# Kernel optimization log

Hardware: AMD Instinct MI355X
Metric: run time of the kernel (lower is better)

## Reference

```python
import jax, jax.numpy as jnp
import numpy as np

N, E, G = 10000, 40000, 128          # nodes, edges, graphs
NF, EF, H, NH, GD, L = 92, 50, 64, 10, 108, 5  # feat dims, hidden, heads, global dim, layers
EPS = 1e-5

def _lrelu(v):
    return jax.nn.leaky_relu(v, 0.2)

def setup_inputs() -> dict:
    key = jax.random.key(0)
    ks = jax.random.split(key, 24)
    def rn(k, shp, s=0.05):
        return jax.random.normal(k, shp, jnp.float32) * s
    return {
        "x": jax.random.normal(ks[0], (N, NF), jnp.float32),
        "edge_index": jax.random.randint(ks[1], (2, E), 0, N, dtype=jnp.int32),
        "edge_attr": jax.random.normal(ks[2], (E, EF), jnp.float32),
        "batch_idx": jnp.sort(jax.random.randint(ks[3], (N,), 0, G, dtype=jnp.int32)),
        "global_features": jax.random.normal(ks[4], (G, GD), jnp.float32),
        "node_W": rn(ks[5], (NF, H)), "node_b": jnp.zeros((H,), jnp.float32),
        "edge_W": rn(ks[6], (EF, H)), "edge_b": jnp.zeros((H,), jnp.float32),
        "conv_W": rn(ks[7], (L, 2 * H, NH * H)),
        "conv_att": rn(ks[8], (L, NH, 2 * H)),
        "conv_b": jnp.zeros((L, H), jnp.float32),
        "conv_gamma": jnp.ones((L, NH), jnp.float32),
        "conv_beta": jnp.zeros((L, NH), jnp.float32),
        "ga_W1": rn(ks[9], (H + GD, H)), "ga_b1": jnp.zeros((H,), jnp.float32),
        "ga_W2": rn(ks[10], (H, 1)), "ga_b2": jnp.zeros((1,), jnp.float32),
        "out_W1": rn(ks[11], (H, H)), "out_b1": jnp.zeros((H,), jnp.float32),
        "out_W2": rn(ks[12], (H, 1)), "out_b2": jnp.zeros((1,), jnp.float32),
    }

def reference(x, edge_index, edge_attr, batch_idx, global_features,
              node_W, node_b, edge_W, edge_b,
              conv_W, conv_att, conv_b, conv_gamma, conv_beta,
              ga_W1, ga_b1, ga_W2, ga_b2, out_W1, out_b1, out_W2, out_b2):
    row, col = edge_index[0], edge_index[1]
    # embeddings
    h = _lrelu(x @ node_W + node_b)            # [N, H]
    ea = _lrelu(edge_attr @ edge_W + edge_b)   # [E, H]
    initial = h
    inv_std = 1.0 / jnp.sqrt(1.0 + EPS)        # DiffGroupNorm eval: running mean=0, var=1
    for i in range(L):
        xi = jnp.concatenate([h[row], ea], axis=-1)               # [E, 2H]
        xj = jnp.concatenate([h[col], ea], axis=-1)
        hi = _lrelu(xi @ conv_W[i]).reshape(E, NH, H)             # [E, NH, H]
        hj = _lrelu(xj @ conv_W[i]).reshape(E, NH, H)
        alpha = jnp.sum(jnp.concatenate([hi, hj], -1) * conv_att[i][None], -1)  # [E, NH]
        alpha = _lrelu(alpha)
        alpha = alpha * inv_std * conv_gamma[i] + conv_beta[i]
        alpha = jax.nn.softmax(alpha, axis=1)                     # softmax over heads
        msg = (hj * alpha[..., None]).reshape(E, NH * H)
        agg = jax.ops.segment_sum(msg, row, num_segments=N).reshape(N, NH, H)
        h_new = agg.mean(axis=1) + conv_b[i]
        h = h + h_new if i > 0 else h_new
    h = h + initial
    # global attention: softmax over nodes within each graph
    g = global_features[batch_idx]                                 # [N, GD]
    s = _lrelu(jnp.concatenate([h, g], -1) @ ga_W1 + ga_b1)
    score = (s @ ga_W2 + ga_b2)[:, 0]                              # [N]
    smax = jax.ops.segment_max(score, batch_idx, num_segments=G)
    ex = jnp.exp(score - smax[batch_idx])
    denom = jax.ops.segment_sum(ex, batch_idx, num_segments=G)
    w = (ex / denom[batch_idx])[:, None]
    h = h * w
    pooled = jax.ops.segment_sum(h, batch_idx, num_segments=G)     # [G, H]
    out = jax.nn.relu(pooled @ out_W1 + out_b1) @ out_W2 + out_b2
    return out[:, 0]
```

## Files before the change

### kernel.cpp

```cpp
#include <hip/hip_runtime.h>
#include <hip/hip_bf16.h>

#define LRELU(v) ((v) > 0.f ? (v) : 0.2f * (v))

__global__ __launch_bounds__(256) void embed_kernel(
    const float* __restrict__ X, const float* __restrict__ W,
    const float* __restrict__ b, float* __restrict__ out, int M, int K) {
  int lane = threadIdx.x & 63;
  int r = blockIdx.x * 4 + (threadIdx.x >> 6);
  if (r >= M) return;
  float acc = b[lane];
  const float* Xr = X + (size_t)r * K;
  for (int k = 0; k < K; ++k) acc = fmaf(Xr[k], W[(size_t)k * 64 + lane], acc);
  acc = LRELU(acc);
  out[(size_t)r * 64 + lane] = acc;
}

template <int ROWS>
__global__ __launch_bounds__(256) void gemm_k64_kernel(
    const float* __restrict__ A, const float* __restrict__ W,
    float* __restrict__ C, int M) {
  const int lane = threadIdx.x & 63;
  const int r0 = (blockIdx.x * 4 + (threadIdx.x >> 6)) * ROWS;
  if (r0 >= M) return;
  float acc[ROWS][10];
#pragma unroll
  for (int r = 0; r < ROWS; ++r)
#pragma unroll
    for (int h = 0; h < 10; ++h) acc[r][h] = 0.f;
  const float* Arow = A + (size_t)r0 * 64;
  for (int k = 0; k < 64; ++k) {
    float w[10];
#pragma unroll
    for (int h = 0; h < 10; ++h) w[h] = W[(size_t)k * 640 + h * 64 + lane];
    float a[ROWS];
#pragma unroll
    for (int r = 0; r < ROWS; ++r) a[r] = Arow[r * 64 + k];
#pragma unroll
    for (int r = 0; r < ROWS; ++r)
#pragma unroll
      for (int h = 0; h < 10; ++h) acc[r][h] = fmaf(a[r], w[h], acc[r][h]);
  }
#pragma unroll
  for (int r = 0; r < ROWS; ++r) {
    float* Crow = C + (size_t)(r0 + r) * 640;
#pragma unroll
    for (int h = 0; h < 10; ++h) Crow[h * 64 + lane] = acc[r][h];
  }
}

__global__ __launch_bounds__(256) void edge_fused_kernel(
    const float* __restrict__ P, const float* __restrict__ ea,
    const float* __restrict__ Wbot,
    const int* __restrict__ row, const int* __restrict__ col,
    const float* __restrict__ att, const float* __restrict__ gamma,
    const float* __restrict__ beta, float* __restrict__ agg, int E_) {
  const int lane = threadIdx.x & 63;
  const int wv = blockIdx.x * 4 + (threadIdx.x >> 6);
  const int e0 = wv * 8;
  if (e0 >= E_) return;

  float eareg[8];
#pragma unroll
  for (int r = 0; r < 8; ++r) {
    int e = e0 + r < E_ ? e0 + r : E_ - 1;
    eareg[r] = ea[(size_t)e * 64 + lane];
  }

  float qacc[8][10];
#pragma unroll
  for (int r = 0; r < 8; ++r)
#pragma unroll
    for (int h = 0; h < 10; ++h) qacc[r][h] = 0.f;
  for (int k = 0; k < 64; ++k) {
    float w[10];
#pragma unroll
    for (int h = 0; h < 10; ++h) w[h] = Wbot[k * 640 + h * 64 + lane];
    float a[8];
#pragma unroll
    for (int r = 0; r < 8; ++r) a[r] = __shfl(eareg[r], k);
#pragma unroll
    for (int r = 0; r < 8; ++r)
#pragma unroll
      for (int h = 0; h < 10; ++h) qacc[r][h] = fmaf(a[r], w[h], qacc[r][h]);
  }

  const float inv_std = 0.9999950000374997f;
#pragma unroll
  for (int r = 0; r < 8; ++r) {
    int e = e0 + r;
    if (e >= E_) break;
    int ri = row[e], ci = col[e];
    const float* Pr = P + (size_t)ri * 640;
    const float* Pc = P + (size_t)ci * 640;
    float hj[10], val[10];
#pragma unroll
    for (int h = 0; h < 10; ++h) {
      float q = qacc[r][h];
      float hi = Pr[h * 64 + lane] + q;
      float hjv = Pc[h * 64 + lane] + q;
      hi = LRELU(hi);
      hjv = LRELU(hjv);
      hj[h] = hjv;
      val[h] = fmaf(hi, att[h * 128 + lane], hjv * att[h * 128 + 64 + lane]);
    }
#pragma unroll
    for (int h = 0; h < 10; ++h) {
      float v = val[h];
#pragma unroll
      for (int off = 32; off; off >>= 1) v += __shfl_xor(v, off);
      val[h] = v;
    }
    float mx = -1e30f;
#pragma unroll
    for (int h = 0; h < 10; ++h) {
      float a = val[h];
      a = LRELU(a);
      a = fmaf(a * inv_std, gamma[h], beta[h]);
      val[h] = a;
      mx = fmaxf(mx, a);
    }
    float ssum = 0.f;
#pragma unroll
    for (int h = 0; h < 10; ++h) {
      float ex = __expf(val[h] - mx);
      val[h] = ex;
      ssum += ex;
    }
    float inv = 1.0f / ssum;
    float m = 0.f;
#pragma unroll
    for (int h = 0; h < 10; ++h) m = fmaf(val[h] * inv, hj[h], m);
    atomicAdd(agg + (size_t)ri * 64 + lane, m);
  }
}

__global__ __launch_bounds__(256) void finalize_kernel(
    float* __restrict__ h, const float* __restrict__ agg,
    const float* __restrict__ b, const float* __restrict__ h0, int mode,
    int total) {
  int idx = blockIdx.x * 256 + threadIdx.x;
  if (idx >= total) return;
  int f = idx & 63;
  float v = fmaf(agg[idx], 0.1f, b[f]);
  if (mode >= 1) v += h[idx];
  if (mode == 2) v += h0[idx];
  h[idx] = v;
}

__global__ __launch_bounds__(256) void score_kernel(
    const float* __restrict__ h, const int* __restrict__ batch,
    const float* __restrict__ gf, const float* __restrict__ W1,
    const float* __restrict__ b1, const float* __restrict__ W2,
    const float* __restrict__ b2, float* __restrict__ score, int N_) {
  int lane = threadIdx.x & 63;
  int n = blockIdx.x * 4 + (threadIdx.x >> 6);
  if (n >= N_) return;
  float acc = b1[lane];
  const float* hn = h + (size_t)n * 64;
#pragma unroll 8
  for (int k = 0; k < 64; ++k) acc = fmaf(hn[k], W1[k * 64 + lane], acc);
  const float* g = gf + (size_t)batch[n] * 108;
#pragma unroll 4
  for (int k = 0; k < 108; ++k) acc = fmaf(g[k], W1[(64 + k) * 64 + lane], acc);
  acc = LRELU(acc);
  float v = acc * W2[lane];
#pragma unroll
  for (int off = 32; off; off >>= 1) v += __shfl_xor(v, off);
  if (lane == 0) score[n] = v + b2[0];
}

__global__ void bounds_kernel(const int* __restrict__ batch,
                              int* __restrict__ start, int N_, int G_) {
  int n = blockIdx.x * blockDim.x + threadIdx.x;
  if (n >= N_) return;
  int b = batch[n];
  int bp = (n == 0) ? -1 : batch[n - 1];
  for (int g = bp + 1; g <= b; ++g) start[g] = n;
  if (n == N_ - 1)
    for (int g = b + 1; g <= G_; ++g) start[g] = N_;
}

__global__ __launch_bounds__(256) void pool_out_kernel(
    const float* __restrict__ h, const float* __restrict__ score,
    const int* __restrict__ start, const float* __restrict__ W1,
    const float* __restrict__ b1, const float* __restrict__ W2,
    const float* __restrict__ b2, float* __restrict__ out) {
  int g = blockIdx.x;
  int s0 = start[g], s1 = start[g + 1];
  int tid = threadIdx.x;
  __shared__ float red[256];
  __shared__ float pool[64];
  __shared__ float sh_smax, sh_denom;
  float lm = -1e30f;
  for (int n = s0 + tid; n < s1; n += 256) lm = fmaxf(lm, score[n]);
  red[tid] = lm;
  __syncthreads();
  for (int off = 128; off; off >>= 1) {
    if (tid < off) red[tid] = fmaxf(red[tid], red[tid + off]);
    __syncthreads();
  }
  if (tid == 0) sh_smax = red[0];
  __syncthreads();
  float smax = sh_smax;
  __syncthreads();
  float ls = 0.f;
  for (int n = s0 + tid; n < s1; n += 256) ls += __expf(score[n] - smax);
  red[tid] = ls;
  __syncthreads();
  for (int off = 128; off; off >>= 1) {
    if (tid < off) red[tid] += red[tid + off];
    __syncthreads();
  }
  if (tid == 0) sh_denom = red[0];
  __syncthreads();
  float denom = sh_denom;
  float invd = denom > 0.f ? 1.0f / denom : 0.f;
  __syncthreads();
  int f = tid & 63, sub = tid >> 6;
  float acc = 0.f;
  for (int n = s0 + sub; n < s1; n += 4)
    acc = fmaf(__expf(score[n] - smax), h[(size_t)n * 64 + f], acc);
  red[tid] = acc;
  __syncthreads();
  if (tid < 64)
    pool[tid] = (red[tid] + red[tid + 64] + red[tid + 128] + red[tid + 192]) * invd;
  __syncthreads();
  if (tid < 64) {
    float a = b1[tid];
#pragma unroll 8
    for (int k = 0; k < 64; ++k) a = fmaf(pool[k], W1[k * 64 + tid], a);
    a = fmaxf(a, 0.f);
    red[tid] = a * W2[tid];
  }
  __syncthreads();
  if (tid == 0) {
    float s = 0.f;
    for (int k = 0; k < 64; ++k) s += red[k];
    out[g] = s + b2[0];
  }
}

extern "C" void kernel_launch(void* const* d_in, const int* in_sizes, int n_in,
                              void* d_out, int out_size, void* d_ws,
                              size_t ws_size, hipStream_t stream) {
  const float* x          = (const float*)d_in[0];
  const int*   edge_index = (const int*)d_in[1];
  const float* edge_attr  = (const float*)d_in[2];
  const int*   batch_idx  = (const int*)d_in[3];
  const float* gf         = (const float*)d_in[4];
  const float* node_W     = (const float*)d_in[5];
  const float* node_b     = (const float*)d_in[6];
  const float* edge_W     = (const float*)d_in[7];
  const float* edge_b     = (const float*)d_in[8];
  const float* conv_W     = (const float*)d_in[9];
  const float* conv_att   = (const float*)d_in[10];
  const float* conv_b     = (const float*)d_in[11];
  const float* conv_gamma = (const float*)d_in[12];
  const float* conv_beta  = (const float*)d_in[13];
  const float* ga_W1      = (const float*)d_in[14];
  const float* ga_b1      = (const float*)d_in[15];
  const float* ga_W2      = (const float*)d_in[16];
  const float* ga_b2      = (const float*)d_in[17];
  const float* out_W1     = (const float*)d_in[18];
  const float* out_b1     = (const float*)d_in[19];
  const float* out_W2     = (const float*)d_in[20];
  const float* out_b2     = (const float*)d_in[21];
  float* out = (float*)d_out;

  const int N = in_sizes[3];
  const int E = in_sizes[2] / 50;
  const int G = in_sizes[4] / 108;
  const int L = 5;

  float* ws = (float*)d_ws;
  float* h    = ws;  ws += (size_t)N * 64;
  float* h0   = ws;  ws += (size_t)N * 64;
  float* ea   = ws;  ws += (size_t)E * 64;
  float* P    = ws;  ws += (size_t)N * 640;
  float* agg  = ws;  ws += (size_t)N * 64;
  float* scr  = ws;  ws += N;
  int* gstart = (int*)ws;

  const int* row = edge_index;
  const int* col = edge_index + E;

  embed_kernel<<<(N + 3) / 4, 256, 0, stream>>>(x, node_W, node_b, h0, N, 92);
  embed_kernel<<<(E + 3) / 4, 256, 0, stream>>>(edge_attr, edge_W, edge_b, ea, E, 50);

  for (int i = 0; i < L; ++i) {
    const float* Wi = conv_W + (size_t)i * 128 * 640;
    gemm_k64_kernel<4><<<(N / 4 + 3) / 4, 256, 0, stream>>>(i == 0 ? h0 : h, Wi, P, N);
    hipMemsetAsync(agg, 0, (size_t)N * 64 * sizeof(float), stream);
    int waves = (E + 7) / 8;
    edge_fused_kernel<<<(waves + 3) / 4, 256, 0, stream>>>(
        P, ea, Wi + 64 * 640, row, col, conv_att + (size_t)i * 1280,
        conv_gamma + i * 10, conv_beta + i * 10, agg, E);
    int mode = (i == 0) ? 0 : (i == L - 1 ? 2 : 1);
    finalize_kernel<<<(N * 64 + 255) / 256, 256, 0, stream>>>(
        h, agg, conv_b + i * 64, h0, mode, N * 64);
  }

  score_kernel<<<(N + 3) / 4, 256, 0, stream>>>(h, batch_idx, gf, ga_W1, ga_b1,
                                                ga_W2, ga_b2, scr, N);
  bounds_kernel<<<(N + 255) / 256, 256, 0, stream>>>(batch_idx, gstart, N, G);
  pool_out_kernel<<<G, 256, 0, stream>>>(h, scr, gstart, out_W1, out_b1, out_W2,
                                         out_b2, out);
}
```

Baseline: 853.0 us.

## Prefetch gathered rows, scalarize wave indices, fold agg zeroing into finalize

The edge kernel now loads row/col indices up front and prefetches the next edge's gathered P rows while the current edge is processed. Edge-feature operands are read directly from memory as scalar-uniform loads instead of being broadcast with cross-lane shuffles. Wave indices are made uniform with readfirstlane in several kernels so address math can run on the scalar unit. The per-layer memset of agg is removed and finalize zeroes agg after reading it, leaving a single memset before the loop. This costs extra registers for the prefetch buffers, which may reduce occupancy.

```diff
diff --git a/kernel.cpp b/kernel.cpp
--- a/kernel.cpp
+++ b/kernel.cpp
@@ -6,12 +6,14 @@
 __global__ __launch_bounds__(256) void embed_kernel(
     const float* __restrict__ X, const float* __restrict__ W,
     const float* __restrict__ b, float* __restrict__ out, int M, int K) {
-  int lane = threadIdx.x & 63;
-  int r = blockIdx.x * 4 + (threadIdx.x >> 6);
+  const int lane = threadIdx.x & 63;
+  const int r =
+      __builtin_amdgcn_readfirstlane(blockIdx.x * 4 + (threadIdx.x >> 6));
   if (r >= M) return;
   float acc = b[lane];
   const float* Xr = X + (size_t)r * K;
-  for (int k = 0; k < K; ++k) acc = fmaf(Xr[k], W[(size_t)k * 64 + lane], acc);
+  const float* Wl = W + lane;
+  for (int k = 0; k < K; ++k) acc = fmaf(Xr[k], Wl[(size_t)k * 64], acc);
   acc = LRELU(acc);
   out[(size_t)r * 64 + lane] = acc;
 }
@@ -21,7 +23,9 @@
     const float* __restrict__ A, const float* __restrict__ W,
     float* __restrict__ C, int M) {
   const int lane = threadIdx.x & 63;
-  const int r0 = (blockIdx.x * 4 + (threadIdx.x >> 6)) * ROWS;
+  const int wv =
+      __builtin_amdgcn_readfirstlane(blockIdx.x * 4 + (threadIdx.x >> 6));
+  const int r0 = wv * ROWS;
   if (r0 >= M) return;
   float acc[ROWS][10];
 #pragma unroll
@@ -29,17 +33,17 @@
 #pragma unroll
     for (int h = 0; h < 10; ++h) acc[r][h] = 0.f;
   const float* Arow = A + (size_t)r0 * 64;
+  const float* Wl = W + lane;
   for (int k = 0; k < 64; ++k) {
     float w[10];
 #pragma unroll
-    for (int h = 0; h < 10; ++h) w[h] = W[(size_t)k * 640 + h * 64 + lane];
-    float a[ROWS];
-#pragma unroll
-    for (int r = 0; r < ROWS; ++r) a[r] = Arow[r * 64 + k];
-#pragma unroll
-    for (int r = 0; r < ROWS; ++r)
-#pragma unroll
-      for (int h = 0; h < 10; ++h) acc[r][h] = fmaf(a[r], w[h], acc[r][h]);
+    for (int h = 0; h < 10; ++h) w[h] = Wl[(size_t)k * 640 + h * 64];
+#pragma unroll
+    for (int r = 0; r < ROWS; ++r) {
+      float a = Arow[r * 64 + k];
+#pragma unroll
+      for (int h = 0; h < 10; ++h) acc[r][h] = fmaf(a, w[h], acc[r][h]);
+    }
   }
 #pragma unroll
   for (int r = 0; r < ROWS; ++r) {
@@ -56,15 +60,18 @@
     const float* __restrict__ att, const float* __restrict__ gamma,
     const float* __restrict__ beta, float* __restrict__ agg, int E_) {
   const int lane = threadIdx.x & 63;
-  const int wv = blockIdx.x * 4 + (threadIdx.x >> 6);
+  const int wv =
+      __builtin_amdgcn_readfirstlane(blockIdx.x * 4 + (threadIdx.x >> 6));
   const int e0 = wv * 8;
   if (e0 >= E_) return;
 
-  float eareg[8];
+  int eix[8], ris[8], cis[8];
 #pragma unroll
   for (int r = 0; r < 8; ++r) {
-    int e = e0 + r < E_ ? e0 + r : E_ - 1;
-    eareg[r] = ea[(size_t)e * 64 + lane];
+    int e = (e0 + r < E_) ? (e0 + r) : (E_ - 1);
+    eix[r] = e;
+    ris[r] = row[e];
+    cis[r] = col[e];
   }
 
   float qacc[8][10];
@@ -72,33 +79,58 @@
   for (int r = 0; r < 8; ++r)
 #pragma unroll
     for (int h = 0; h < 10; ++h) qacc[r][h] = 0.f;
+
+  const float* Wl = Wbot + lane;
   for (int k = 0; k < 64; ++k) {
     float w[10];
 #pragma unroll
-    for (int h = 0; h < 10; ++h) w[h] = Wbot[k * 640 + h * 64 + lane];
-    float a[8];
-#pragma unroll
-    for (int r = 0; r < 8; ++r) a[r] = __shfl(eareg[r], k);
-#pragma unroll
-    for (int r = 0; r < 8; ++r)
-#pragma unroll
-      for (int h = 0; h < 10; ++h) qacc[r][h] = fmaf(a[r], w[h], qacc[r][h]);
+    for (int h = 0; h < 10; ++h) w[h] = Wl[k * 640 + h * 64];
+#pragma unroll
+    for (int r = 0; r < 8; ++r) {
+      float a = ea[(size_t)eix[r] * 64 + k];
+#pragma unroll
+      for (int h = 0; h < 10; ++h) qacc[r][h] = fmaf(a, w[h], qacc[r][h]);
+    }
   }
 
   const float inv_std = 0.9999950000374997f;
+
+  float prb[10], pcb[10];
+  {
+    const float* Pr = P + (size_t)ris[0] * 640 + lane;
+    const float* Pc = P + (size_t)cis[0] * 640 + lane;
+#pragma unroll
+    for (int h = 0; h < 10; ++h) {
+      prb[h] = Pr[h * 64];
+      pcb[h] = Pc[h * 64];
+    }
+  }
+
 #pragma unroll
   for (int r = 0; r < 8; ++r) {
     int e = e0 + r;
     if (e >= E_) break;
-    int ri = row[e], ci = col[e];
-    const float* Pr = P + (size_t)ri * 640;
-    const float* Pc = P + (size_t)ci * 640;
+    float pr[10], pc[10];
+#pragma unroll
+    for (int h = 0; h < 10; ++h) {
+      pr[h] = prb[h];
+      pc[h] = pcb[h];
+    }
+    if (r + 1 < 8) {
+      const float* Pr = P + (size_t)ris[r + 1] * 640 + lane;
+      const float* Pc = P + (size_t)cis[r + 1] * 640 + lane;
+#pragma unroll
+      for (int h = 0; h < 10; ++h) {
+        prb[h] = Pr[h * 64];
+        pcb[h] = Pc[h * 64];
+      }
+    }
     float hj[10], val[10];
 #pragma unroll
     for (int h = 0; h < 10; ++h) {
       float q = qacc[r][h];
-      float hi = Pr[h * 64 + lane] + q;
-      float hjv = Pc[h * 64 + lane] + q;
+      float hi = pr[h] + q;
+      float hjv = pc[h] + q;
       hi = LRELU(hi);
       hjv = LRELU(hjv);
       hj[h] = hjv;
@@ -131,18 +163,18 @@
     float m = 0.f;
 #pragma unroll
     for (int h = 0; h < 10; ++h) m = fmaf(val[h] * inv, hj[h], m);
-    atomicAdd(agg + (size_t)ri * 64 + lane, m);
+    atomicAdd(agg + (size_t)ris[r] * 64 + lane, m);
   }
 }
 
 __global__ __launch_bounds__(256) void finalize_kernel(
-    float* __restrict__ h, const float* __restrict__ agg,
-    const float* __restrict__ b, const float* __restrict__ h0, int mode,
-    int total) {
+    float* __restrict__ h, float* __restrict__ agg, const float* __restrict__ b,
+    const float* __restrict__ h0, int mode, int total) {
   int idx = blockIdx.x * 256 + threadIdx.x;
   if (idx >= total) return;
   int f = idx & 63;
   float v = fmaf(agg[idx], 0.1f, b[f]);
+  agg[idx] = 0.f;
   if (mode >= 1) v += h[idx];
   if (mode == 2) v += h0[idx];
   h[idx] = v;
@@ -153,16 +185,19 @@
     const float* __restrict__ gf, const float* __restrict__ W1,
     const float* __restrict__ b1, const float* __restrict__ W2,
     const float* __restrict__ b2, float* __restrict__ score, int N_) {
-  int lane = threadIdx.x & 63;
-  int n = blockIdx.x * 4 + (threadIdx.x >> 6);
+  const int lane = threadIdx.x & 63;
+  const int n =
+      __builtin_amdgcn_readfirstlane(blockIdx.x * 4 + (threadIdx.x >> 6));
   if (n >= N_) return;
   float acc = b1[lane];
   const float* hn = h + (size_t)n * 64;
+  const float* W1l = W1 + lane;
 #pragma unroll 8
-  for (int k = 0; k < 64; ++k) acc = fmaf(hn[k], W1[k * 64 + lane], acc);
-  const float* g = gf + (size_t)batch[n] * 108;
+  for (int k = 0; k < 64; ++k) acc = fmaf(hn[k], W1l[k * 64], acc);
+  const int bn = batch[n];
+  const float* g = gf + (size_t)bn * 108;
 #pragma unroll 4
-  for (int k = 0; k < 108; ++k) acc = fmaf(g[k], W1[(64 + k) * 64 + lane], acc);
+  for (int k = 0; k < 108; ++k) acc = fmaf(g[k], W1l[(64 + k) * 64], acc);
   acc = LRELU(acc);
   float v = acc * W2[lane];
 #pragma unroll
@@ -224,7 +259,8 @@
   red[tid] = acc;
   __syncthreads();
   if (tid < 64)
-    pool[tid] = (red[tid] + red[tid + 64] + red[tid + 128] + red[tid + 192]) * invd;
+    pool[tid] =
+        (red[tid] + red[tid + 64] + red[tid + 128] + red[tid + 192]) * invd;
   __syncthreads();
   if (tid < 64) {
     float a = b1[tid];
@@ -286,12 +322,14 @@
   const int* col = edge_index + E;
 
   embed_kernel<<<(N + 3) / 4, 256, 0, stream>>>(x, node_W, node_b, h0, N, 92);
-  embed_kernel<<<(E + 3) / 4, 256, 0, stream>>>(edge_attr, edge_W, edge_b, ea, E, 50);
+  embed_kernel<<<(E + 3) / 4, 256, 0, stream>>>(edge_attr, edge_W, edge_b, ea,
+                                                E, 50);
+  hipMemsetAsync(agg, 0, (size_t)N * 64 * sizeof(float), stream);
 
   for (int i = 0; i < L; ++i) {
     const float* Wi = conv_W + (size_t)i * 128 * 640;
-    gemm_k64_kernel<4><<<(N / 4 + 3) / 4, 256, 0, stream>>>(i == 0 ? h0 : h, Wi, P, N);
-    hipMemsetAsync(agg, 0, (size_t)N * 64 * sizeof(float), stream);
+    gemm_k64_kernel<4><<<(N / 4 + 3) / 4, 256, 0, stream>>>(i == 0 ? h0 : h,
+                                                            Wi, P, N);
     int waves = (E + 7) / 8;
     edge_fused_kernel<<<(waves + 3) / 4, 256, 0, stream>>>(
         P, ea, Wi + 64 * 640, row, col, conv_att + (size_t)i * 1280,
```

Result: faster. 780.4 us (-8.5%).
